# Kernel optimization log

Hardware: AMD Instinct MI355X
Metric: run time of the kernel (lower is better)

The kernel has to match this reference:

```python
import jax, jax.numpy as jnp
import numpy as np

N_NODES = 10000
N_EDGES = 320000
HIDDEN = 256          # hidden_feat -> dim of gcn output x
MLP_IN = 2 * HIDDEN   # concat(src, dst)
OUT_FEATURES = 10


def setup_inputs() -> dict:
    key = jax.random.key(0)
    k_x, k_e, k_w1, k_w2 = jax.random.split(key, 4)
    x = jax.random.normal(k_x, (N_NODES, HIDDEN), dtype=jnp.float32)
    edge_index = jax.random.randint(k_e, (2, N_EDGES), 0, N_NODES, dtype=jnp.int64)
    # ClassifierMLP2(2*hidden_feat, out_features): Linear -> ReLU -> Linear -> log_softmax
    W1 = jax.random.normal(k_w1, (MLP_IN, HIDDEN), dtype=jnp.float32) * 0.02
    b1 = jnp.zeros((HIDDEN,), dtype=jnp.float32)
    W2 = jax.random.normal(k_w2, (HIDDEN, OUT_FEATURES), dtype=jnp.float32) * 0.02
    b2 = jnp.zeros((OUT_FEATURES,), dtype=jnp.float32)
    return {"x": x, "edge_index": edge_index, "W1": W1, "b1": b1, "W2": W2, "b2": b2}


def reference(x, edge_index, W1, b1, W2, b2):
    # mix_node_features(..., node_feat_mixing='cat'):
    # gather source/target node features per edge and concatenate -> [E, 2*H]
    src, dst = edge_index[0], edge_index[1]
    edges_x = jnp.concatenate([x[src], x[dst]], axis=1)  # [E, 2H]
    # ClassifierMLP2 forward
    h = jax.nn.relu(edges_x @ W1 + b1)                   # [E, H]
    logits = h @ W2 + b2                                 # [E, C]
    return jax.nn.log_softmax(logits, axis=-1)
```

## Files before the change

### kernel.cpp

```cpp
#include <hip/hip_runtime.h>

#define E_TOTAL 320000
#define NNODES  10000
#define HID     256
#define NCLS    10

typedef __attribute__((ext_vector_type(4))) float f32x4;
typedef __attribute__((ext_vector_type(2))) float f32x2;
typedef __attribute__((ext_vector_type(4))) unsigned int u32x4;
typedef __attribute__((ext_vector_type(8))) __bf16 bf16x8;
typedef __attribute__((ext_vector_type(8))) unsigned short u16x8;

static __device__ __forceinline__ unsigned short f2bf(float f) {
  unsigned u = __builtin_bit_cast(unsigned, f);
  u += 0x7fffu + ((u >> 16) & 1u);
  return (unsigned short)(u >> 16);
}

__global__ void k_pack(const float* __restrict__ x,
                       const float* __restrict__ W1,
                       const float* __restrict__ W2,
                       unsigned short* __restrict__ xbf,
                       unsigned short* __restrict__ w1f,
                       unsigned short* __restrict__ w2f) {
  int b = blockIdx.x, tid = threadIdx.x;
  if (b < 1250) {
    int i = b * 256 + tid;
    const f32x4* s = (const f32x4*)x + (size_t)i * 2;
    f32x4 a = s[0], c = s[1];
    u16x8 o;
    o[0]=f2bf(a[0]); o[1]=f2bf(a[1]); o[2]=f2bf(a[2]); o[3]=f2bf(a[3]);
    o[4]=f2bf(c[0]); o[5]=f2bf(c[1]); o[6]=f2bf(c[2]); o[7]=f2bf(c[3]);
    *((u16x8*)xbf + i) = o;
  } else if (b < 1314) {
    int gid = (b - 1250) * 256 + tid;
    int l = gid & 63, kk = (gid >> 6) & 7, cb = (gid >> 9) & 15, half = gid >> 13;
    int kbase = half * 256 + kk * 32 + (l >> 4) * 8;
    int col = cb * 16 + (l & 15);
    u16x8 o;
#pragma unroll
    for (int j = 0; j < 8; ++j) o[j] = f2bf(W1[(size_t)(kbase + j) * HID + col]);
    *((u16x8*)w1f + gid) = o;
  } else {
    int gid = (b - 1314) * 256 + tid;
    int l = gid & 63, kk = gid >> 6;
    int kbase = kk * 32 + (l >> 4) * 8;
    int c = l & 15;
    u16x8 o;
#pragma unroll
    for (int j = 0; j < 8; ++j)
      o[j] = (c < NCLS) ? f2bf(W2[(size_t)(kbase + j) * NCLS + c]) : (unsigned short)0;
    *((u16x8*)w2f + gid) = o;
  }
}

__global__ __launch_bounds__(256, 3) void k_prep(
    const unsigned short* __restrict__ xbf,
    const unsigned short* __restrict__ w1f,
    const float* __restrict__ b1,
    unsigned char* __restrict__ Yf8)
{
  __shared__ __align__(16) unsigned short ldsA[2][32 * 64];

  const int tid  = threadIdx.x;
  const int lane = tid & 63;
  const int wv   = tid >> 6;
  const int n0   = blockIdx.x * 32;
  const int half = blockIdx.y;
  const int l15  = lane & 15;
  const int lhi  = lane >> 4;

  f32x4 acc[2][4] = {};

  auto stageA = [&](int kb, int buf) {
    int col0 = kb * 64;
    int r = wv * 8 + (lane >> 3);
    int gr = n0 + r; if (gr > NNODES - 1) gr = NNODES - 1;
    int usrc = (lane & 7) ^ (r & 7);
    const unsigned short* g = xbf + (size_t)gr * HID + col0 + usrc * 8;
    unsigned short* lp = &ldsA[buf][(wv * 8) * 64];
    __builtin_amdgcn_global_load_lds(
        (const __attribute__((address_space(1))) unsigned int*)g,
        (__attribute__((address_space(3))) unsigned int*)lp,
        16, 0, 0);
  };

  stageA(0, 0);

  for (int kb = 0; kb < 4; ++kb) {
    int buf = kb & 1;
    __syncthreads();
    if (kb < 3) stageA(kb + 1, buf ^ 1);

    bf16x8 bfr[2][4];
#pragma unroll
    for (int ks = 0; ks < 2; ++ks)
#pragma unroll
      for (int n = 0; n < 4; ++n) {
        int cb = wv * 4 + n;
        int kk = kb * 2 + ks;
        int f = (half * 16 + cb) * 8 + kk;
        bfr[ks][n] = *(const bf16x8*)(w1f + ((size_t)f * 64 + lane) * 8);
      }

#pragma unroll
    for (int ks = 0; ks < 2; ++ks) {
      bf16x8 afr[2];
#pragma unroll
      for (int m = 0; m < 2; ++m) {
        int row = m * 16 + l15;
        int boff = row * 128 + ((ks * 64 + lhi * 16) ^ ((row & 7) << 4));
        afr[m] = *(const bf16x8*)((const char*)&ldsA[buf][0] + boff);
      }
#pragma unroll
      for (int m = 0; m < 2; ++m)
#pragma unroll
        for (int n = 0; n < 4; ++n)
          acc[m][n] = __builtin_amdgcn_mfma_f32_16x16x32_bf16(afr[m], bfr[ks][n], acc[m][n], 0, 0, 0);
    }
  }

  float b1v[4];
#pragma unroll
  for (int n = 0; n < 4; ++n) b1v[n] = (half == 0) ? b1[wv * 64 + n * 16 + l15] : 0.f;

#pragma unroll
  for (int m = 0; m < 2; ++m)
#pragma unroll
    for (int n = 0; n < 4; ++n) {
      int col = wv * 64 + n * 16 + l15;
      int pos = ((col >> 3) & 3) * 64 + ((col >> 5) << 3) + (col & 7);
#pragma unroll
      for (int r = 0; r < 4; ++r) {
        int row = m * 16 + lhi * 4 + r;
        int gr = n0 + row;
        if (gr < NNODES) {
          float v = acc[m][n][r] + b1v[n];
          int pk = __builtin_amdgcn_cvt_pk_fp8_f32(v, v, 0, false);
          Yf8[(size_t)gr * 512 + half * 256 + pos] = (unsigned char)(pk & 0xff);
        }
      }
    }
}

__global__ __launch_bounds__(256, 4) void k_edge(
    const int* __restrict__ ei,
    const unsigned char* __restrict__ Yf8,
    const unsigned short* __restrict__ w2f,
    const float* __restrict__ b2,
    float* __restrict__ out)
{
  __shared__ __align__(16) unsigned short ldsW[4096];

  const int tid  = threadIdx.x;
  const int lane = tid & 63;
  const int wv   = tid >> 6;
  const int e0   = blockIdx.x * 64;
  const int l15  = lane & 15;
  const int lhi  = lane >> 4;

  int edge = e0 + wv * 16 + l15;
  int src = ei[edge];
  int dst = ei[E_TOTAL + edge];

  {
    const u16x8* s = (const u16x8*)w2f;
    u16x8* d = (u16x8*)ldsW;
    d[tid] = s[tid];
    d[tid + 256] = s[tid + 256];
  }
  __syncthreads();

  const u32x4* q1 = (const u32x4*)(Yf8 + (size_t)src * 512 + lhi * 64);
  const u32x4* q2 = (const u32x4*)(Yf8 + (size_t)dst * 512 + 256 + lhi * 64);
  u32x4 ya[4], yb[4];
#pragma unroll
  for (int i = 0; i < 4; ++i) { ya[i] = q1[i]; yb[i] = q2[i]; }

  f32x4 lg = {0.f, 0.f, 0.f, 0.f};
#pragma unroll
  for (int kk = 0; kk < 8; ++kk) {
    bf16x8 bw = *(const bf16x8*)(ldsW + kk * 512 + lane * 8);
    unsigned a0 = ya[kk >> 1][(kk & 1) * 2], a1 = ya[kk >> 1][(kk & 1) * 2 + 1];
    unsigned c0 = yb[kk >> 1][(kk & 1) * 2], c1 = yb[kk >> 1][(kk & 1) * 2 + 1];
    f32x2 A0 = __builtin_amdgcn_cvt_pk_f32_fp8(a0, false);
    f32x2 A1 = __builtin_amdgcn_cvt_pk_f32_fp8(a0, true);
    f32x2 A2 = __builtin_amdgcn_cvt_pk_f32_fp8(a1, false);
    f32x2 A3 = __builtin_amdgcn_cvt_pk_f32_fp8(a1, true);
    f32x2 B0 = __builtin_amdgcn_cvt_pk_f32_fp8(c0, false);
    f32x2 B1 = __builtin_amdgcn_cvt_pk_f32_fp8(c0, true);
    f32x2 B2 = __builtin_amdgcn_cvt_pk_f32_fp8(c1, false);
    f32x2 B3 = __builtin_amdgcn_cvt_pk_f32_fp8(c1, true);
    bf16x8 hh;
    hh[0] = (__bf16)fmaxf(A0[0] + B0[0], 0.f);
    hh[1] = (__bf16)fmaxf(A0[1] + B0[1], 0.f);
    hh[2] = (__bf16)fmaxf(A1[0] + B1[0], 0.f);
    hh[3] = (__bf16)fmaxf(A1[1] + B1[1], 0.f);
    hh[4] = (__bf16)fmaxf(A2[0] + B2[0], 0.f);
    hh[5] = (__bf16)fmaxf(A2[1] + B2[1], 0.f);
    hh[6] = (__bf16)fmaxf(A3[0] + B3[0], 0.f);
    hh[7] = (__bf16)fmaxf(A3[1] + B3[1], 0.f);
    lg = __builtin_amdgcn_mfma_f32_16x16x32_bf16(hh, bw, lg, 0, 0, 0);
  }

  bool valid = (l15 < NCLS);
  float bias = valid ? b2[l15] : 0.f;
#pragma unroll
  for (int r = 0; r < 4; ++r) {
    float v = lg[r] + bias;
    float mv = valid ? v : -1e30f;
#pragma unroll
    for (int s = 1; s < 16; s <<= 1) mv = fmaxf(mv, __shfl_xor(mv, s, 64));
    float ev = valid ? __expf(v - mv) : 0.f;
    float sv = ev;
#pragma unroll
    for (int s = 1; s < 16; s <<= 1) sv += __shfl_xor(sv, s, 64);
    float res = v - mv - __logf(sv);
    if (valid) out[(size_t)(e0 + wv * 16 + lhi * 4 + r) * NCLS + l15] = res;
  }
}

extern "C" void kernel_launch(void* const* d_in, const int* in_sizes, int n_in,
                              void* d_out, int out_size, void* d_ws, size_t ws_size,
                              hipStream_t stream) {
  const float* x  = (const float*)d_in[0];
  const int*   ei = (const int*)d_in[1];
  const float* W1 = (const float*)d_in[2];
  const float* b1 = (const float*)d_in[3];
  const float* W2 = (const float*)d_in[4];
  const float* b2 = (const float*)d_in[5];
  float* out = (float*)d_out;

  unsigned short* xbf = (unsigned short*)d_ws;
  unsigned short* w1f = xbf + (size_t)NNODES * HID;
  unsigned short* w2f = w1f + (size_t)131072;
  unsigned char*  Yf8 = (unsigned char*)(w2f + 4096);

  k_pack<<<1316, 256, 0, stream>>>(x, W1, W2, xbf, w1f, w2f);
  k_prep<<<dim3((NNODES + 31) / 32, 2), 256, 0, stream>>>(xbf, w1f, b1, Yf8);
  k_edge<<<E_TOTAL / 64, 256, 0, stream>>>(ei, Yf8, w2f, b2, out);
}
```

Baseline: 52.75 us.

## Stage edge gathers through LDS with coalesced 16-lane row loads

The edge kernel now loads src/dst indices into LDS once per block. Each node row is then gathered by 16 lanes reading contiguous 16-byte chunks, so whole 256-byte rows are read coalesced instead of each lane pulling 64 bytes. The rows go into a swizzled LDS tile that the MFMA fragment reads pull from. The Y layout is simplified to natural column order to match. This costs 32KB+ of LDS and an extra barrier, and occupancy drops to 3 blocks.

```diff
diff --git a/kernel.cpp b/kernel.cpp
--- a/kernel.cpp
+++ b/kernel.cpp
@@ -8,6 +8,7 @@
 typedef __attribute__((ext_vector_type(4))) float f32x4;
 typedef __attribute__((ext_vector_type(2))) float f32x2;
 typedef __attribute__((ext_vector_type(4))) unsigned int u32x4;
+typedef __attribute__((ext_vector_type(2))) unsigned int u32x2;
 typedef __attribute__((ext_vector_type(8))) __bf16 bf16x8;
 typedef __attribute__((ext_vector_type(8))) unsigned short u16x8;
 
@@ -129,7 +130,6 @@
 #pragma unroll
     for (int n = 0; n < 4; ++n) {
       int col = wv * 64 + n * 16 + l15;
-      int pos = ((col >> 3) & 3) * 64 + ((col >> 5) << 3) + (col & 7);
 #pragma unroll
       for (int r = 0; r < 4; ++r) {
         int row = m * 16 + lhi * 4 + r;
@@ -137,13 +137,13 @@
         if (gr < NNODES) {
           float v = acc[m][n][r] + b1v[n];
           int pk = __builtin_amdgcn_cvt_pk_fp8_f32(v, v, 0, false);
-          Yf8[(size_t)gr * 512 + half * 256 + pos] = (unsigned char)(pk & 0xff);
+          Yf8[(size_t)gr * 512 + half * 256 + col] = (unsigned char)(pk & 0xff);
         }
       }
     }
 }
 
-__global__ __launch_bounds__(256, 4) void k_edge(
+__global__ __launch_bounds__(256, 3) void k_edge(
     const int* __restrict__ ei,
     const unsigned char* __restrict__ Yf8,
     const unsigned short* __restrict__ w2f,
@@ -151,6 +151,8 @@
     float* __restrict__ out)
 {
   __shared__ __align__(16) unsigned short ldsW[4096];
+  __shared__ __align__(16) unsigned char  ldsD[2][64][256];
+  __shared__ int ldsIdx[2][64];
 
   const int tid  = threadIdx.x;
   const int lane = tid & 63;
@@ -159,38 +161,55 @@
   const int l15  = lane & 15;
   const int lhi  = lane >> 4;
 
-  int edge = e0 + wv * 16 + l15;
-  int src = ei[edge];
-  int dst = ei[E_TOTAL + edge];
-
   {
     const u16x8* s = (const u16x8*)w2f;
     u16x8* d = (u16x8*)ldsW;
     d[tid] = s[tid];
     d[tid + 256] = s[tid + 256];
   }
+  if (tid < 128) {
+    int s = tid >> 6, e = tid & 63;
+    ldsIdx[s][e] = ei[s * E_TOTAL + e0 + e];
+  }
   __syncthreads();
 
-  const u32x4* q1 = (const u32x4*)(Yf8 + (size_t)src * 512 + lhi * 64);
-  const u32x4* q2 = (const u32x4*)(Yf8 + (size_t)dst * 512 + 256 + lhi * 64);
-  u32x4 ya[4], yb[4];
-#pragma unroll
-  for (int i = 0; i < 4; ++i) { ya[i] = q1[i]; yb[i] = q2[i]; }
-
+  const int ch = tid & 15;
+  const int eb = tid >> 4;
+  u32x4 gbuf[2][4];
+#pragma unroll
+  for (int s = 0; s < 2; ++s)
+#pragma unroll
+    for (int k = 0; k < 4; ++k) {
+      int e = k * 16 + eb;
+      int node = ldsIdx[s][e];
+      gbuf[s][k] = *(const u32x4*)(Yf8 + (size_t)node * 512 + s * 256 + ch * 16);
+    }
+#pragma unroll
+  for (int s = 0; s < 2; ++s)
+#pragma unroll
+    for (int k = 0; k < 4; ++k) {
+      int e = k * 16 + eb;
+      *(u32x4*)&ldsD[s][e][((ch ^ (e & 15)) * 16)] = gbuf[s][k];
+    }
+  __syncthreads();
+
+  const int r = wv * 16 + l15;
   f32x4 lg = {0.f, 0.f, 0.f, 0.f};
 #pragma unroll
   for (int kk = 0; kk < 8; ++kk) {
     bf16x8 bw = *(const bf16x8*)(ldsW + kk * 512 + lane * 8);
-    unsigned a0 = ya[kk >> 1][(kk & 1) * 2], a1 = ya[kk >> 1][(kk & 1) * 2 + 1];
-    unsigned c0 = yb[kk >> 1][(kk & 1) * 2], c1 = yb[kk >> 1][(kk & 1) * 2 + 1];
-    f32x2 A0 = __builtin_amdgcn_cvt_pk_f32_fp8(a0, false);
-    f32x2 A1 = __builtin_amdgcn_cvt_pk_f32_fp8(a0, true);
-    f32x2 A2 = __builtin_amdgcn_cvt_pk_f32_fp8(a1, false);
-    f32x2 A3 = __builtin_amdgcn_cvt_pk_f32_fp8(a1, true);
-    f32x2 B0 = __builtin_amdgcn_cvt_pk_f32_fp8(c0, false);
-    f32x2 B1 = __builtin_amdgcn_cvt_pk_f32_fp8(c0, true);
-    f32x2 B2 = __builtin_amdgcn_cvt_pk_f32_fp8(c1, false);
-    f32x2 B3 = __builtin_amdgcn_cvt_pk_f32_fp8(c1, true);
+    int c0 = kk * 2 + (lhi >> 1);
+    int off = (lhi & 1) * 8;
+    u32x2 A = *(const u32x2*)&ldsD[0][r][((c0 ^ l15) * 16) + off];
+    u32x2 B = *(const u32x2*)&ldsD[1][r][((c0 ^ l15) * 16) + off];
+    f32x2 A0 = __builtin_amdgcn_cvt_pk_f32_fp8(A[0], false);
+    f32x2 A1 = __builtin_amdgcn_cvt_pk_f32_fp8(A[0], true);
+    f32x2 A2 = __builtin_amdgcn_cvt_pk_f32_fp8(A[1], false);
+    f32x2 A3 = __builtin_amdgcn_cvt_pk_f32_fp8(A[1], true);
+    f32x2 B0 = __builtin_amdgcn_cvt_pk_f32_fp8(B[0], false);
+    f32x2 B1 = __builtin_amdgcn_cvt_pk_f32_fp8(B[0], true);
+    f32x2 B2 = __builtin_amdgcn_cvt_pk_f32_fp8(B[1], false);
+    f32x2 B3 = __builtin_amdgcn_cvt_pk_f32_fp8(B[1], true);
     bf16x8 hh;
     hh[0] = (__bf16)fmaxf(A0[0] + B0[0], 0.f);
     hh[1] = (__bf16)fmaxf(A0[1] + B0[1], 0.f);
@@ -206,8 +225,8 @@
   bool valid = (l15 < NCLS);
   float bias = valid ? b2[l15] : 0.f;
 #pragma unroll
-  for (int r = 0; r < 4; ++r) {
-    float v = lg[r] + bias;
+  for (int rr = 0; rr < 4; ++rr) {
+    float v = lg[rr] + bias;
     float mv = valid ? v : -1e30f;
 #pragma unroll
     for (int s = 1; s < 16; s <<= 1) mv = fmaxf(mv, __shfl_xor(mv, s, 64));
@@ -216,7 +235,7 @@
 #pragma unroll
     for (int s = 1; s < 16; s <<= 1) sv += __shfl_xor(sv, s, 64);
     float res = v - mv - __logf(sv);
-    if (valid) out[(size_t)(e0 + wv * 16 + lhi * 4 + r) * NCLS + l15] = res;
+    if (valid) out[(size_t)(e0 + wv * 16 + lhi * 4 + rr) * NCLS + l15] = res;
   }
 }
 
```

Result: slower. 54.43 us (+3.2%).

## Sort edges by source node via counting sort before edge MLP kernel

Applied to the files above, without the earlier changes.

Adds a histogram, single-block prefix scan, and atomic scatter pass that reorders edges by source node, so the edge kernel reads consecutive edges sharing a source row and gets better cache locality on the fp8 node table. Output is written back through a permutation index. The price is four extra launches plus a memset, atomics contention, and scattered output writes. The edge lists reuse the xbf workspace region after k_prep has finished with it.

```diff
diff --git a/kernel.cpp b/kernel.cpp
--- a/kernel.cpp
+++ b/kernel.cpp
@@ -143,8 +143,48 @@
     }
 }
 
+__global__ void k_hist(const int* __restrict__ ei, int* __restrict__ cnt) {
+  int e = blockIdx.x * 256 + threadIdx.x;
+  atomicAdd(&cnt[ei[e]], 1);
+}
+
+__global__ __launch_bounds__(1024) void k_scan(int* __restrict__ cnt) {
+  __shared__ int part[1024];
+  int t = threadIdx.x;
+  int v[10];
+  int s = 0;
+  if (t < 1000) {
+#pragma unroll
+    for (int j = 0; j < 10; ++j) { v[j] = cnt[t * 10 + j]; s += v[j]; }
+  }
+  part[t] = s;
+  __syncthreads();
+  for (int off = 1; off < 1024; off <<= 1) {
+    int x = (t >= off) ? part[t - off] : 0;
+    __syncthreads();
+    part[t] += x;
+    __syncthreads();
+  }
+  if (t < 1000) {
+    int run = part[t] - s;
+#pragma unroll
+    for (int j = 0; j < 10; ++j) { cnt[t * 10 + j] = run; run += v[j]; }
+  }
+}
+
+__global__ void k_scatter(const int* __restrict__ ei, int* __restrict__ cnt,
+                          int* __restrict__ se, int* __restrict__ de,
+                          int* __restrict__ pe) {
+  int e = blockIdx.x * 256 + threadIdx.x;
+  int s = ei[e], d = ei[E_TOTAL + e];
+  int pos = atomicAdd(&cnt[s], 1);
+  se[pos] = s; de[pos] = d; pe[pos] = e;
+}
+
 __global__ __launch_bounds__(256, 4) void k_edge(
-    const int* __restrict__ ei,
+    const int* __restrict__ se,
+    const int* __restrict__ de,
+    const int* __restrict__ pe,
     const unsigned char* __restrict__ Yf8,
     const unsigned short* __restrict__ w2f,
     const float* __restrict__ b2,
@@ -160,8 +200,8 @@
   const int lhi  = lane >> 4;
 
   int edge = e0 + wv * 16 + l15;
-  int src = ei[edge];
-  int dst = ei[E_TOTAL + edge];
+  int src = se[edge];
+  int dst = de[edge];
 
   {
     const u16x8* s = (const u16x8*)w2f;
@@ -216,7 +256,10 @@
 #pragma unroll
     for (int s = 1; s < 16; s <<= 1) sv += __shfl_xor(sv, s, 64);
     float res = v - mv - __logf(sv);
-    if (valid) out[(size_t)(e0 + wv * 16 + lhi * 4 + r) * NCLS + l15] = res;
+    if (valid) {
+      int eo = pe[e0 + wv * 16 + lhi * 4 + r];
+      out[(size_t)eo * NCLS + l15] = res;
+    }
   }
 }
 
@@ -231,12 +274,21 @@
   const float* b2 = (const float*)d_in[5];
   float* out = (float*)d_out;
 
-  unsigned short* xbf = (unsigned short*)d_ws;
-  unsigned short* w1f = xbf + (size_t)NNODES * HID;
-  unsigned short* w2f = w1f + (size_t)131072;
-  unsigned char*  Yf8 = (unsigned char*)(w2f + 4096);
+  char* ws = (char*)d_ws;
+  unsigned short* xbf = (unsigned short*)ws;
+  unsigned short* w1f = (unsigned short*)(ws + 5120000);
+  unsigned short* w2f = (unsigned short*)(ws + 5382144);
+  unsigned char*  Yf8 = (unsigned char*)(ws + 5390336);
+  int* se  = (int*)(ws + 0);
+  int* de  = (int*)(ws + 1280000);
+  int* pe  = (int*)(ws + 2560000);
+  int* cnt = (int*)(ws + 3840000);
 
   k_pack<<<1316, 256, 0, stream>>>(x, W1, W2, xbf, w1f, w2f);
   k_prep<<<dim3((NNODES + 31) / 32, 2), 256, 0, stream>>>(xbf, w1f, b1, Yf8);
-  k_edge<<<E_TOTAL / 64, 256, 0, stream>>>(ei, Yf8, w2f, b2, out);
-}
+  hipMemsetAsync(cnt, 0, 40000, stream);
+  k_hist<<<E_TOTAL / 256, 256, 0, stream>>>(ei, cnt);
+  k_scan<<<1, 1024, 0, stream>>>(cnt);
+  k_scatter<<<E_TOTAL / 256, 256, 0, stream>>>(ei, cnt, se, de, pe);
+  k_edge<<<E_TOTAL / 64, 256, 0, stream>>>(se, de, pe, Yf8, w2f, b2, out);
+}
```

Measured after the change: 110.7 us. +109.8%, slower.

## Fuse x bf16 conversion into prep GEMM and use fp8 MFMA for edge layer

Applied to the files above, without the earlier changes.

The separate pass that converts x to bf16 in workspace is removed. k_prep now loads fp32 x directly, converts it in registers and writes bf16 into LDS with register double-buffering, which saves a global round trip. The edge kernel's second layer now packs the ReLU hidden activations and W2 (pre-scaled by 16) into fp8 and uses the fp8 MFMA, rescaling the logits by 1/16 afterwards. This adds precision loss on both the activations and W2, and k_prep loses its async global-to-LDS loads.

```diff
diff --git a/kernel.cpp b/kernel.cpp
--- a/kernel.cpp
+++ b/kernel.cpp
@@ -8,6 +8,7 @@
 typedef __attribute__((ext_vector_type(4))) float f32x4;
 typedef __attribute__((ext_vector_type(2))) float f32x2;
 typedef __attribute__((ext_vector_type(4))) unsigned int u32x4;
+typedef __attribute__((ext_vector_type(2))) unsigned int u32x2;
 typedef __attribute__((ext_vector_type(8))) __bf16 bf16x8;
 typedef __attribute__((ext_vector_type(8))) unsigned short u16x8;
 
@@ -17,23 +18,13 @@
   return (unsigned short)(u >> 16);
 }
 
-__global__ void k_pack(const float* __restrict__ x,
-                       const float* __restrict__ W1,
+__global__ void k_pack(const float* __restrict__ W1,
                        const float* __restrict__ W2,
-                       unsigned short* __restrict__ xbf,
                        unsigned short* __restrict__ w1f,
-                       unsigned short* __restrict__ w2f) {
+                       unsigned long long* __restrict__ w2f8) {
   int b = blockIdx.x, tid = threadIdx.x;
-  if (b < 1250) {
-    int i = b * 256 + tid;
-    const f32x4* s = (const f32x4*)x + (size_t)i * 2;
-    f32x4 a = s[0], c = s[1];
-    u16x8 o;
-    o[0]=f2bf(a[0]); o[1]=f2bf(a[1]); o[2]=f2bf(a[2]); o[3]=f2bf(a[3]);
-    o[4]=f2bf(c[0]); o[5]=f2bf(c[1]); o[6]=f2bf(c[2]); o[7]=f2bf(c[3]);
-    *((u16x8*)xbf + i) = o;
-  } else if (b < 1314) {
-    int gid = (b - 1250) * 256 + tid;
+  if (b < 64) {
+    int gid = b * 256 + tid;
     int l = gid & 63, kk = (gid >> 6) & 7, cb = (gid >> 9) & 15, half = gid >> 13;
     int kbase = half * 256 + kk * 32 + (l >> 4) * 8;
     int col = cb * 16 + (l & 15);
@@ -42,20 +33,25 @@
     for (int j = 0; j < 8; ++j) o[j] = f2bf(W1[(size_t)(kbase + j) * HID + col]);
     *((u16x8*)w1f + gid) = o;
   } else {
-    int gid = (b - 1314) * 256 + tid;
+    int gid = (b - 64) * 256 + tid;
     int l = gid & 63, kk = gid >> 6;
     int kbase = kk * 32 + (l >> 4) * 8;
     int c = l & 15;
-    u16x8 o;
+    float v[8];
 #pragma unroll
     for (int j = 0; j < 8; ++j)
-      o[j] = (c < NCLS) ? f2bf(W2[(size_t)(kbase + j) * NCLS + c]) : (unsigned short)0;
-    *((u16x8*)w2f + gid) = o;
+      v[j] = (c < NCLS) ? W2[(size_t)(kbase + j) * NCLS + c] * 16.f : 0.f;
+    int lo = __builtin_amdgcn_cvt_pk_fp8_f32(v[0], v[1], 0, false);
+    lo = __builtin_amdgcn_cvt_pk_fp8_f32(v[2], v[3], lo, true);
+    int hi = __builtin_amdgcn_cvt_pk_fp8_f32(v[4], v[5], 0, false);
+    hi = __builtin_amdgcn_cvt_pk_fp8_f32(v[6], v[7], hi, true);
+    u32x2 p = {(unsigned)lo, (unsigned)hi};
+    w2f8[gid] = __builtin_bit_cast(unsigned long long, p);
   }
 }
 
 __global__ __launch_bounds__(256, 3) void k_prep(
-    const unsigned short* __restrict__ xbf,
+    const float* __restrict__ x,
     const unsigned short* __restrict__ w1f,
     const float* __restrict__ b1,
     unsigned char* __restrict__ Yf8)
@@ -70,36 +66,43 @@
   const int l15  = lane & 15;
   const int lhi  = lane >> 4;
 
+  const int lr  = wv * 8 + (lane >> 3);
+  int gr = n0 + lr; if (gr > NNODES - 1) gr = NNODES - 1;
+  const float* xrow = x + (size_t)gr * HID + (lane & 7) * 8;
+  const int wboff = lr * 128 + (((lane & 7) ^ (lr & 7)) * 16);
+
   f32x4 acc[2][4] = {};
 
-  auto stageA = [&](int kb, int buf) {
-    int col0 = kb * 64;
-    int r = wv * 8 + (lane >> 3);
-    int gr = n0 + r; if (gr > NNODES - 1) gr = NNODES - 1;
-    int usrc = (lane & 7) ^ (r & 7);
-    const unsigned short* g = xbf + (size_t)gr * HID + col0 + usrc * 8;
-    unsigned short* lp = &ldsA[buf][(wv * 8) * 64];
-    __builtin_amdgcn_global_load_lds(
-        (const __attribute__((address_space(1))) unsigned int*)g,
-        (__attribute__((address_space(3))) unsigned int*)lp,
-        16, 0, 0);
+  auto loadX = [&](int kb, f32x4& va, f32x4& vb) {
+    const float* g = xrow + kb * 64;
+    va = *(const f32x4*)g;
+    vb = *(const f32x4*)(g + 4);
   };
-
-  stageA(0, 0);
+  auto writeX = [&](int buf, const f32x4& va, const f32x4& vb) {
+    u16x8 o;
+#pragma unroll
+    for (int j = 0; j < 4; ++j) { o[j] = f2bf(va[j]); o[j + 4] = f2bf(vb[j]); }
+    *(u16x8*)((char*)&ldsA[buf][0] + wboff) = o;
+  };
+
+  f32x4 ca, cb2;
+  loadX(0, ca, cb2);
+  writeX(0, ca, cb2);
+  __syncthreads();
 
   for (int kb = 0; kb < 4; ++kb) {
     int buf = kb & 1;
-    __syncthreads();
-    if (kb < 3) stageA(kb + 1, buf ^ 1);
+    f32x4 na, nb;
+    if (kb < 3) loadX(kb + 1, na, nb);
 
     bf16x8 bfr[2][4];
 #pragma unroll
     for (int ks = 0; ks < 2; ++ks)
 #pragma unroll
       for (int n = 0; n < 4; ++n) {
-        int cb = wv * 4 + n;
+        int cbk = wv * 4 + n;
         int kk = kb * 2 + ks;
-        int f = (half * 16 + cb) * 8 + kk;
+        int f = (half * 16 + cbk) * 8 + kk;
         bfr[ks][n] = *(const bf16x8*)(w1f + ((size_t)f * 64 + lane) * 8);
       }
 
@@ -118,6 +121,9 @@
         for (int n = 0; n < 4; ++n)
           acc[m][n] = __builtin_amdgcn_mfma_f32_16x16x32_bf16(afr[m], bfr[ks][n], acc[m][n], 0, 0, 0);
     }
+
+    if (kb < 3) writeX(buf ^ 1, na, nb);
+    __syncthreads();
   }
 
   float b1v[4];
@@ -133,11 +139,11 @@
 #pragma unroll
       for (int r = 0; r < 4; ++r) {
         int row = m * 16 + lhi * 4 + r;
-        int gr = n0 + row;
-        if (gr < NNODES) {
+        int g2 = n0 + row;
+        if (g2 < NNODES) {
           float v = acc[m][n][r] + b1v[n];
           int pk = __builtin_amdgcn_cvt_pk_fp8_f32(v, v, 0, false);
-          Yf8[(size_t)gr * 512 + half * 256 + pos] = (unsigned char)(pk & 0xff);
+          Yf8[(size_t)g2 * 512 + half * 256 + pos] = (unsigned char)(pk & 0xff);
         }
       }
     }
@@ -146,11 +152,11 @@
 __global__ __launch_bounds__(256, 4) void k_edge(
     const int* __restrict__ ei,
     const unsigned char* __restrict__ Yf8,
-    const unsigned short* __restrict__ w2f,
+    const unsigned long long* __restrict__ w2f8,
     const float* __restrict__ b2,
     float* __restrict__ out)
 {
-  __shared__ __align__(16) unsigned short ldsW[4096];
+  __shared__ __align__(16) unsigned long long ldsW64[512];
 
   const int tid  = threadIdx.x;
   const int lane = tid & 63;
@@ -163,12 +169,8 @@
   int src = ei[edge];
   int dst = ei[E_TOTAL + edge];
 
-  {
-    const u16x8* s = (const u16x8*)w2f;
-    u16x8* d = (u16x8*)ldsW;
-    d[tid] = s[tid];
-    d[tid + 256] = s[tid + 256];
-  }
+  ldsW64[tid] = w2f8[tid];
+  ldsW64[tid + 256] = w2f8[tid + 256];
   __syncthreads();
 
   const u32x4* q1 = (const u32x4*)(Yf8 + (size_t)src * 512 + lhi * 64);
@@ -177,37 +179,35 @@
 #pragma unroll
   for (int i = 0; i < 4; ++i) { ya[i] = q1[i]; yb[i] = q2[i]; }
 
+  const f32x2 zero2 = {0.f, 0.f};
   f32x4 lg = {0.f, 0.f, 0.f, 0.f};
 #pragma unroll
   for (int kk = 0; kk < 8; ++kk) {
-    bf16x8 bw = *(const bf16x8*)(ldsW + kk * 512 + lane * 8);
+    long bop = (long)ldsW64[kk * 64 + lane];
     unsigned a0 = ya[kk >> 1][(kk & 1) * 2], a1 = ya[kk >> 1][(kk & 1) * 2 + 1];
     unsigned c0 = yb[kk >> 1][(kk & 1) * 2], c1 = yb[kk >> 1][(kk & 1) * 2 + 1];
-    f32x2 A0 = __builtin_amdgcn_cvt_pk_f32_fp8(a0, false);
-    f32x2 A1 = __builtin_amdgcn_cvt_pk_f32_fp8(a0, true);
-    f32x2 A2 = __builtin_amdgcn_cvt_pk_f32_fp8(a1, false);
-    f32x2 A3 = __builtin_amdgcn_cvt_pk_f32_fp8(a1, true);
-    f32x2 B0 = __builtin_amdgcn_cvt_pk_f32_fp8(c0, false);
-    f32x2 B1 = __builtin_amdgcn_cvt_pk_f32_fp8(c0, true);
-    f32x2 B2 = __builtin_amdgcn_cvt_pk_f32_fp8(c1, false);
-    f32x2 B3 = __builtin_amdgcn_cvt_pk_f32_fp8(c1, true);
-    bf16x8 hh;
-    hh[0] = (__bf16)fmaxf(A0[0] + B0[0], 0.f);
-    hh[1] = (__bf16)fmaxf(A0[1] + B0[1], 0.f);
-    hh[2] = (__bf16)fmaxf(A1[0] + B1[0], 0.f);
-    hh[3] = (__bf16)fmaxf(A1[1] + B1[1], 0.f);
-    hh[4] = (__bf16)fmaxf(A2[0] + B2[0], 0.f);
-    hh[5] = (__bf16)fmaxf(A2[1] + B2[1], 0.f);
-    hh[6] = (__bf16)fmaxf(A3[0] + B3[0], 0.f);
-    hh[7] = (__bf16)fmaxf(A3[1] + B3[1], 0.f);
-    lg = __builtin_amdgcn_mfma_f32_16x16x32_bf16(hh, bw, lg, 0, 0, 0);
+    f32x2 s0 = __builtin_amdgcn_cvt_pk_f32_fp8(a0, false) + __builtin_amdgcn_cvt_pk_f32_fp8(c0, false);
+    f32x2 s1 = __builtin_amdgcn_cvt_pk_f32_fp8(a0, true)  + __builtin_amdgcn_cvt_pk_f32_fp8(c0, true);
+    f32x2 s2 = __builtin_amdgcn_cvt_pk_f32_fp8(a1, false) + __builtin_amdgcn_cvt_pk_f32_fp8(c1, false);
+    f32x2 s3 = __builtin_amdgcn_cvt_pk_f32_fp8(a1, true)  + __builtin_amdgcn_cvt_pk_f32_fp8(c1, true);
+    s0 = __builtin_elementwise_max(s0, zero2);
+    s1 = __builtin_elementwise_max(s1, zero2);
+    s2 = __builtin_elementwise_max(s2, zero2);
+    s3 = __builtin_elementwise_max(s3, zero2);
+    int lo = __builtin_amdgcn_cvt_pk_fp8_f32(s0[0], s0[1], 0, false);
+    lo = __builtin_amdgcn_cvt_pk_fp8_f32(s1[0], s1[1], lo, true);
+    int hi = __builtin_amdgcn_cvt_pk_fp8_f32(s2[0], s2[1], 0, false);
+    hi = __builtin_amdgcn_cvt_pk_fp8_f32(s3[0], s3[1], hi, true);
+    u32x2 ap = {(unsigned)lo, (unsigned)hi};
+    long aop = __builtin_bit_cast(long, ap);
+    lg = __builtin_amdgcn_mfma_f32_16x16x32_fp8_fp8(aop, bop, lg, 0, 0, 0);
   }
 
   bool valid = (l15 < NCLS);
   float bias = valid ? b2[l15] : 0.f;
 #pragma unroll
   for (int r = 0; r < 4; ++r) {
-    float v = lg[r] + bias;
+    float v = lg[r] * 0.0625f + bias;
     float mv = valid ? v : -1e30f;
 #pragma unroll
     for (int s = 1; s < 16; s <<= 1) mv = fmaxf(mv, __shfl_xor(mv, s, 64));
@@ -231,12 +231,12 @@
   const float* b2 = (const float*)d_in[5];
   float* out = (float*)d_out;
 
-  unsigned short* xbf = (unsigned short*)d_ws;
-  unsigned short* w1f = xbf + (size_t)NNODES * HID;
-  unsigned short* w2f = w1f + (size_t)131072;
-  unsigned char*  Yf8 = (unsigned char*)(w2f + 4096);
-
-  k_pack<<<1316, 256, 0, stream>>>(x, W1, W2, xbf, w1f, w2f);
-  k_prep<<<dim3((NNODES + 31) / 32, 2), 256, 0, stream>>>(xbf, w1f, b1, Yf8);
-  k_edge<<<E_TOTAL / 64, 256, 0, stream>>>(ei, Yf8, w2f, b2, out);
-}
+  char* ws = (char*)d_ws;
+  unsigned short* w1f = (unsigned short*)ws;
+  unsigned long long* w2f8 = (unsigned long long*)(ws + 262144);
+  unsigned char* Yf8 = (unsigned char*)(ws + 266240);
+
+  k_pack<<<66, 256, 0, stream>>>(W1, W2, w1f, w2f8);
+  k_prep<<<dim3((NNODES + 31) / 32, 2), 256, 0, stream>>>(x, w1f, b1, Yf8);
+  k_edge<<<E_TOTAL / 64, 256, 0, stream>>>(ei, Yf8, w2f8, b2, out);
+}
```

Measured after the change: 54.24 us. 2.8% more time.
